# Kernel tuning notes

Hardware: AMD Instinct MI355X
Metric: run time of the kernel (lower is better)

Reference implementation:

```python
import jax, jax.numpy as jnp
import numpy as np

NUM_IN_CAPS = 1152   # 32 * 6 * 6
NUM_OUT_CAPS = 10
IN_DIM = 8
OUT_DIM = 16
ROUTING_ITERS = 3
EPS = 1e-8


def squash(s, axis=-1):
    # squash(s) = ||s||^2/(1+||s||^2) * s/||s||
    sq = jnp.sum(s * s, axis=axis, keepdims=True)
    norm = jnp.sqrt(sq + EPS)
    return (sq / (1.0 + sq)) * (s / norm)


def setup_inputs() -> dict:
    key = jax.random.key(0)
    ks = jax.random.split(key, 6)
    B = 512
    inp = jax.random.uniform(ks[0], (B, 1, 28, 28), dtype=jnp.float32)
    # conv params (He-ish scale)
    conv1_w = jax.random.normal(ks[1], (256, 1, 9, 9), dtype=jnp.float32) * 0.05
    conv1_b = jnp.zeros((256,), dtype=jnp.float32)
    conv2_w = jax.random.normal(ks[2], (256, 256, 9, 9), dtype=jnp.float32) * 0.01
    conv2_b = jnp.zeros((256,), dtype=jnp.float32)
    # capsule transform weights: [in_caps, out_caps, in_dim, out_dim]
    cap_W = jax.random.normal(ks[3], (NUM_IN_CAPS, NUM_OUT_CAPS, IN_DIM, OUT_DIM), dtype=jnp.float32) * 0.05
    return {"input": inp, "conv1_w": conv1_w, "conv1_b": conv1_b,
            "conv2_w": conv2_w, "conv2_b": conv2_b, "cap_W": cap_W}


def _conv(x, w, b, stride):
    y = jax.lax.conv_general_dilated(
        x, w, window_strides=(stride, stride), padding='VALID',
        dimension_numbers=('NCHW', 'OIHW', 'NCHW'))
    return y + b[None, :, None, None]


def capsnet_forward(input, conv1_w, conv1_b, conv2_w, conv2_b, cap_W):
    B = input.shape[0]
    h = jax.nn.relu(_conv(input, conv1_w, conv1_b, 1))   # [B,256,20,20]
    h = _conv(h, conv2_w, conv2_b, 2)                    # [B,256,6,6]
    # torch.transpose(output, 1, -1): [B,C,H,W] -> [B,W,H,C], then view(B,1152,8)
    u = jnp.transpose(h, (0, 3, 2, 1)).reshape(B, NUM_IN_CAPS, IN_DIM)
    # predicted output vectors u_hat: [B, i, j, q]
    u_hat = jnp.einsum('bip,ijpq->bijq', u, cap_W)
    # dynamic routing
    b_ij = jnp.zeros((B, NUM_IN_CAPS, NUM_OUT_CAPS), dtype=u_hat.dtype)
    v = None
    for _ in range(ROUTING_ITERS):
        c = jax.nn.softmax(b_ij, axis=2)                 # coupling over output caps
        s = jnp.einsum('bij,bijq->bjq', c, u_hat)        # [B, j, q]
        v = squash(s)                                    # [B, j, q]
        b_ij = b_ij + jnp.einsum('bijq,bjq->bij', u_hat, v)
    return v  # [B, 10, 16]


def reference(input, conv1_w, conv1_b, conv2_w, conv2_b, cap_W):
    return capsnet_forward(input, conv1_w, conv1_b, conv2_w, conv2_b, cap_W)
```

## Files before the change

kernel.cpp:

```cpp
#include <hip/hip_runtime.h>
#include <hip/hip_bf16.h>

typedef __attribute__((ext_vector_type(8))) short bf16x8;
typedef __attribute__((ext_vector_type(4))) float f32x4;

static __device__ __forceinline__ unsigned short f2bf(float x) {
    __hip_bfloat16 h = __float2bfloat16(x);
    return *(unsigned short*)&h;
}
static __device__ __forceinline__ float bflo(unsigned int w) { return __uint_as_float(w << 16); }
static __device__ __forceinline__ float bfhi(unsigned int w) { return __uint_as_float(w & 0xffff0000u); }
static __device__ __forceinline__ float bf1(unsigned short u) { return __uint_as_float(((unsigned int)u) << 16); }

typedef __attribute__((address_space(1))) const void gvoid;
typedef __attribute__((address_space(3))) void lvoid;
static __device__ __forceinline__ void gl_lds16(const void* g, void* l) {
    __builtin_amdgcn_global_load_lds((gvoid*)g, (lvoid*)l, 16, 0, 0);
}

#define PART_FLOATS 4718592

__global__ __launch_bounds__(320) void conv1_k(const float* __restrict__ in,
                                               const float* __restrict__ w,
                                               const float* __restrict__ bias,
                                               unsigned short* __restrict__ h1n) {
    int blk = blockIdx.x;
    int b = blk >> 4;
    int c0 = (blk & 15) * 16;
    __shared__ float img[784];
    __shared__ float wl[16 * 81];
    __shared__ float bl[16];
    __shared__ unsigned short tr[20 * 328];
    int tid = threadIdx.x;
    for (int t = tid; t < 784; t += 320) img[t] = in[b * 784 + t];
    for (int t = tid; t < 1296; t += 320) wl[t] = w[c0 * 81 + t];
    if (tid < 16) bl[tid] = bias[c0 + tid];
    __syncthreads();

    int co = tid / 20, oy = tid % 20;
    float wr[81];
#pragma unroll
    for (int k = 0; k < 81; k++) wr[k] = wl[co * 81 + k];
    float acc[20];
    float bv = bl[co];
#pragma unroll
    for (int ox = 0; ox < 20; ox++) acc[ox] = bv;

#pragma unroll
    for (int ky = 0; ky < 9; ky++) {
        const float* rp = &img[(oy + ky) * 28];
        float r[28];
#pragma unroll
        for (int v = 0; v < 7; v++) {
            float4 t4 = ((const float4*)rp)[v];
            r[v * 4 + 0] = t4.x; r[v * 4 + 1] = t4.y;
            r[v * 4 + 2] = t4.z; r[v * 4 + 3] = t4.w;
        }
#pragma unroll
        for (int kx = 0; kx < 9; kx++) {
            float wv = wr[ky * 9 + kx];
#pragma unroll
            for (int ox = 0; ox < 20; ox++) acc[ox] += r[ox + kx] * wv;
        }
    }
#pragma unroll
    for (int ox = 0; ox < 20; ox++)
        tr[oy * 328 + ox * 16 + co] = f2bf(fmaxf(acc[ox], 0.f));
    __syncthreads();
    for (int g = tid; g < 800; g += 320) {
        int p = g >> 1, half = g & 1;
        uint4 v = *(uint4*)&tr[(p / 20) * 328 + (p % 20) * 16 + half * 8];
        *(uint4*)&h1n[(b * 400 + p) * 256 + c0 + half * 8] = v;
    }
}

__global__ __launch_bounds__(256) void wt2_k(const float* __restrict__ w2,
                                             unsigned short* __restrict__ Wt2) {
    int cout = blockIdx.x;
    int tid = threadIdx.x;
    __shared__ unsigned short lw[256 * 84];
    lw[tid * 84 + 81] = 0; lw[tid * 84 + 82] = 0; lw[tid * 84 + 83] = 0;
    const float4* src = (const float4*)(w2 + (size_t)cout * 20736);
    for (int t = tid; t < 5184; t += 256) {
        float4 v = src[t];
        int flat = t * 4;
#pragma unroll
        for (int e = 0; e < 4; e++) {
            int f = flat + e;
            int cin = f / 81, kk = f - cin * 81;
            float x = (e == 0) ? v.x : (e == 1) ? v.y : (e == 2) ? v.z : v.w;
            lw[cin * 84 + kk] = f2bf(x);
        }
    }
    __syncthreads();
    int kko = tid >> 7, c2 = (tid & 127) * 2;
    for (int base = 0; base < 84; base += 2) {
        int kk = base + kko;
        unsigned int val = (unsigned int)lw[c2 * 84 + kk]
                         | ((unsigned int)lw[(c2 + 1) * 84 + kk] << 16);
        *(unsigned int*)&Wt2[(size_t)kk * 65536 + cout * 256 + c2] = val;
    }
}

__global__ __launch_bounds__(256) void wcap_k(const float* __restrict__ W,
                                              unsigned short* __restrict__ Wb) {
    int idx4 = blockIdx.x * 256 + threadIdx.x;
    float4 v = *(const float4*)&W[(size_t)idx4 * 4];
    unsigned int lo = (unsigned int)f2bf(v.x) | ((unsigned int)f2bf(v.y) << 16);
    unsigned int hi = (unsigned int)f2bf(v.z) | ((unsigned int)f2bf(v.w) << 16);
    uint2 pk; pk.x = lo; pk.y = hi;
    *(uint2*)&Wb[(size_t)idx4 * 4] = pk;
}

__global__ __launch_bounds__(256) void conv2_k(const unsigned short* __restrict__ h1n,
                                               const unsigned short* __restrict__ Wt2,
                                               const float* __restrict__ bias,
                                               float* __restrict__ u,
                                               float* __restrict__ part1,
                                               float* __restrict__ part23) {
    __shared__ unsigned short sA[2][128 * 64];
    __shared__ unsigned short sB[2][128 * 64];
    int tid = threadIdx.x;
    int m0 = blockIdx.x * 128;
    int n0 = blockIdx.y * 128;
    int slice = blockIdx.z;
    int ks = slice * 21;

    int wv = tid >> 6, lane = tid & 63;
    int wm = wv >> 1, wn = wv & 1;
    int lr = lane & 15, quad = lane >> 4;

    int lrow = lane >> 3, lslot = lane & 7;
    int kcoff = (lslot ^ lrow) * 8;
    int aG[4], bG[4];
#pragma unroll
    for (int t = 0; t < 4; t++) {
        int r = wv * 32 + t * 8 + lrow;
        int R = m0 + r;
        int b = R / 36, m = R % 36;
        int oy = m / 6, ox = m % 6;
        aG[t] = b * 102400 + oy * 10240 + ox * 512 + kcoff;
        bG[t] = (n0 + r) * 256 + kcoff;
    }

    f32x4 acc[4][4];
#pragma unroll
    for (int i = 0; i < 4; i++)
#pragma unroll
        for (int j = 0; j < 4; j++) acc[i][j] = (f32x4){0.f, 0.f, 0.f, 0.f};

    auto stage = [&](int buf, int rr) {
        int kk = ks + (rr >> 2), cr = rr & 3;
        int ky = kk / 9, kx = kk % 9;
        int aoff = ky * 5120 + kx * 256 + cr * 64;
        int boff = kk * 65536 + cr * 64;
        unsigned short* dA = &sA[buf][wv * 2048];
        unsigned short* dB = &sB[buf][wv * 2048];
#pragma unroll
        for (int t = 0; t < 4; t++)
            gl_lds16(h1n + aG[t] + aoff, dA + t * 512);
#pragma unroll
        for (int t = 0; t < 4; t++)
            gl_lds16(Wt2 + bG[t] + boff, dB + t * 512);
    };

    stage(0, 0);
    __syncthreads();

    int cur = 0;
#pragma unroll 1
    for (int rr = 0; rr < 84; rr++) {
        if (rr < 83) stage(cur ^ 1, rr + 1);
        const unsigned short* pA = &sA[cur][0];
        const unsigned short* pB = &sB[cur][0];
#pragma unroll
        for (int s = 0; s < 2; s++) {
            bf16x8 af[4], bf[4];
#pragma unroll
            for (int i = 0; i < 4; i++) {
                int arow = wm * 64 + i * 16 + lr;
                af[i] = *(bf16x8*)&pA[arow * 64 + 8 * ((s * 4 + quad) ^ (lr & 7))];
            }
#pragma unroll
            for (int j = 0; j < 4; j++) {
                int brow = wn * 64 + j * 16 + lr;
                bf[j] = *(bf16x8*)&pB[brow * 64 + 8 * ((s * 4 + quad) ^ (lr & 7))];
            }
#pragma unroll
            for (int i = 0; i < 4; i++)
#pragma unroll
                for (int j = 0; j < 4; j++)
                    acc[i][j] = __builtin_amdgcn_mfma_f32_16x16x32_bf16(
                        af[i], bf[j], acc[i][j], 0, 0, 0);
        }
        __syncthreads();
        cur ^= 1;
    }

    float* dst = (slice == 0) ? u : ((slice == 1) ? part1 : part23 + (size_t)(slice - 2) * PART_FLOATS);
#pragma unroll
    for (int j = 0; j < 4; j++) {
        int col = n0 + wn * 64 + j * 16 + lr;
        float bv = (slice == 0) ? bias[col] : 0.f;
#pragma unroll
        for (int i = 0; i < 4; i++) {
#pragma unroll
            for (int rg = 0; rg < 4; rg++) {
                int RR = m0 + wm * 64 + i * 16 + quad * 4 + rg;
                int bb = RR / 36, mm = RR % 36;
                int oyy = mm / 6, oxx = mm % 6;
                dst[bb * 9216 + oxx * 1536 + oyy * 256 + col] = acc[i][j][rg] + bv;
            }
        }
    }
}

__global__ __launch_bounds__(256) void uhat_k(const float* __restrict__ u,
                                              const float* __restrict__ p1,
                                              const float* __restrict__ p23,
                                              const unsigned short* __restrict__ Wb,
                                              unsigned short* __restrict__ uhat) {
    int i0 = blockIdx.x * 64;
    int b0 = blockIdx.y * 8;
    __shared__ float ul[8 * 576];
    __shared__ unsigned short wl[64 * 130];
    int tid = threadIdx.x;

    for (int t = tid; t < 1024; t += 256) {
        int bb = t >> 7, rq = t & 127;
        int r = rq * 4;
        size_t gidx = (size_t)(b0 + bb) * 9216 + i0 * 8 + r;
        float4 a = *(const float4*)&u[gidx];
        float4 x = *(const float4*)&p1[gidx];
        float4 y = *(const float4*)&p23[gidx];
        float4 z = *(const float4*)&p23[PART_FLOATS + gidx];
        float* d = &ul[bb * 576 + (r >> 3) * 9 + (r & 7)];
        d[0] = a.x + x.x + y.x + z.x;
        d[1] = a.y + x.y + y.y + z.y;
        d[2] = a.z + x.z + y.z + z.z;
        d[3] = a.w + x.w + y.w + z.w;
    }

    int il = tid & 63, g = tid >> 6;
    for (int j = 0; j < 10; j++) {
        __syncthreads();
        for (int t = tid; t < 4096; t += 256) {
            int li = t >> 6, cp = t & 63;
            *(unsigned int*)&wl[li * 130 + cp * 2] =
                *(const unsigned int*)&Wb[(size_t)(i0 + li) * 1280 + j * 128 + cp * 2];
        }
        __syncthreads();
#pragma unroll 1
        for (int bb = 0; bb < 8; bb++) {
            float ur[8];
#pragma unroll
            for (int p = 0; p < 8; p++) ur[p] = ul[bb * 576 + il * 9 + p];
            float a[4];
#pragma unroll
            for (int k = 0; k < 4; k++) {
                int q = g * 4 + k;
                float s = 0.f;
#pragma unroll
                for (int p = 0; p < 8; p++) s += ur[p] * bf1(wl[il * 130 + p * 16 + q]);
                a[k] = s;
            }
            unsigned int lo = (unsigned int)f2bf(a[0]) | ((unsigned int)f2bf(a[1]) << 16);
            unsigned int hi = (unsigned int)f2bf(a[2]) | ((unsigned int)f2bf(a[3]) << 16);
            uint2 pk; pk.x = lo; pk.y = hi;
            *(uint2*)&uhat[((size_t)(b0 + bb) * 10 + j) * 18432 + (size_t)(i0 + il) * 16 + g * 4] = pk;
        }
    }
}

__global__ __launch_bounds__(256) void route_k(const unsigned short* __restrict__ uhat,
                                               float* __restrict__ out) {
    int b = blockIdx.x;
    int tid = threadIdx.x;
    int w = tid >> 6, lane = tid & 63;
    int ig = lane >> 2, qh = lane & 3;
    __shared__ float b_sh[1152 * 10];
    __shared__ float s_red[4 * 160];
    __shared__ float v_sh[160];
    __shared__ float sc_sh[10];
    const unsigned short* ub = uhat + (size_t)b * 184320;

    float v_ln[10][4];

    auto finish = [&](float sp[10][4]) {
#pragma unroll
        for (int j = 0; j < 10; j++)
#pragma unroll
            for (int k = 0; k < 4; k++) {
                float t = sp[j][k];
                t += __shfl_xor(t, 4);
                t += __shfl_xor(t, 8);
                t += __shfl_xor(t, 16);
                t += __shfl_xor(t, 32);
                sp[j][k] = t;
            }
        if (ig == 0) {
#pragma unroll
            for (int j = 0; j < 10; j++) {
                f32x4 v4 = {sp[j][0], sp[j][1], sp[j][2], sp[j][3]};
                *(f32x4*)&s_red[w * 160 + j * 16 + qh * 4] = v4;
            }
        }
        __syncthreads();
        if (tid < 160) {
            float s = s_red[tid] + s_red[160 + tid] + s_red[320 + tid] + s_red[480 + tid];
            s_red[tid] = s;
        }
        __syncthreads();
        if (tid < 10) {
            float sq = 0.f;
#pragma unroll
            for (int q = 0; q < 16; q++) { float x = s_red[tid * 16 + q]; sq += x * x; }
            float norm = sqrtf(sq + 1e-8f);
            sc_sh[tid] = (sq / (1.0f + sq)) / norm;
        }
        __syncthreads();
        if (tid < 160) v_sh[tid] = s_red[tid] * sc_sh[tid >> 4];
        __syncthreads();
#pragma unroll
        for (int j = 0; j < 10; j++) {
            f32x4 v4 = *(const f32x4*)&v_sh[j * 16 + qh * 4];
            v_ln[j][0] = v4[0]; v_ln[j][1] = v4[1]; v_ln[j][2] = v4[2]; v_ln[j][3] = v4[3];
        }
        __syncthreads();
    };

    {
        float sp[10][4];
#pragma unroll
        for (int j = 0; j < 10; j++)
#pragma unroll
            for (int k = 0; k < 4; k++) sp[j][k] = 0.f;
#pragma unroll 2
        for (int r = 0; r < 18; r++) {
            int i = r * 64 + w * 16 + ig;
            const unsigned short* up = ub + (size_t)i * 16 + qh * 4;
            uint2 uh[10];
#pragma unroll
            for (int j = 0; j < 10; j++) uh[j] = *(const uint2*)(up + (size_t)j * 18432);
#pragma unroll
            for (int j = 0; j < 10; j++) {
                sp[j][0] += 0.1f * bflo(uh[j].x);
                sp[j][1] += 0.1f * bfhi(uh[j].x);
                sp[j][2] += 0.1f * bflo(uh[j].y);
                sp[j][3] += 0.1f * bfhi(uh[j].y);
            }
        }
        finish(sp);
    }

#pragma unroll 1
    for (int pass = 0; pass < 2; pass++) {
        bool first = (pass == 0);
        float sp[10][4];
#pragma unroll
        for (int j = 0; j < 10; j++)
#pragma unroll
            for (int k = 0; k < 4; k++) sp[j][k] = 0.f;
#pragma unroll 2
        for (int r = 0; r < 18; r++) {
            int i = r * 64 + w * 16 + ig;
            const unsigned short* up = ub + (size_t)i * 16 + qh * 4;
            uint2 uh[10];
#pragma unroll
            for (int j = 0; j < 10; j++) uh[j] = *(const uint2*)(up + (size_t)j * 18432);
            float d[10];
#pragma unroll
            for (int j = 0; j < 10; j++) {
                d[j] = bflo(uh[j].x) * v_ln[j][0] + bfhi(uh[j].x) * v_ln[j][1]
                     + bflo(uh[j].y) * v_ln[j][2] + bfhi(uh[j].y) * v_ln[j][3];
            }
#pragma unroll
            for (int j = 0; j < 10; j++) {
                d[j] += __shfl_xor(d[j], 1);
                d[j] += __shfl_xor(d[j], 2);
            }
            float bn[10];
            if (first) {
#pragma unroll
                for (int j = 0; j < 10; j++) bn[j] = d[j];
#pragma unroll
                for (int j = 0; j < 10; j++)
                    if (qh == (j & 3)) b_sh[i * 10 + j] = bn[j];
            } else {
#pragma unroll
                for (int j = 0; j < 10; j++) bn[j] = b_sh[i * 10 + j] + d[j];
            }
            float m = bn[0];
#pragma unroll
            for (int j = 1; j < 10; j++) m = fmaxf(m, bn[j]);
            float e[10], sum = 0.f;
#pragma unroll
            for (int j = 0; j < 10; j++) { e[j] = __expf(bn[j] - m); sum += e[j]; }
            float inv = 1.f / sum;
#pragma unroll
            for (int j = 0; j < 10; j++) {
                float c = e[j] * inv;
                sp[j][0] += c * bflo(uh[j].x);
                sp[j][1] += c * bfhi(uh[j].x);
                sp[j][2] += c * bflo(uh[j].y);
                sp[j][3] += c * bfhi(uh[j].y);
            }
        }
        finish(sp);
    }

    if (tid < 160) out[b * 160 + tid] = v_sh[tid];
}

extern "C" void kernel_launch(void* const* d_in, const int* in_sizes, int n_in,
                              void* d_out, int out_size, void* d_ws, size_t ws_size,
                              hipStream_t stream) {
    const float* input = (const float*)d_in[0];
    const float* c1w = (const float*)d_in[1];
    const float* c1b = (const float*)d_in[2];
    const float* c2w = (const float*)d_in[3];
    const float* c2b = (const float*)d_in[4];
    const float* capW = (const float*)d_in[5];
    float* out = (float*)d_out;

    const size_t U_OFF = 0;
    const size_t P1_OFF = 18874368;
    const size_t WB_OFF = 37748736;
    const size_t B_OFF = 43122688;
    const size_t WT2_BYTES = (size_t)84 * 65536 * 2;
    const size_t H1N_BYTES = 104857600;
    const size_t PART_BYTES = (size_t)PART_FLOATS * 4;
    const size_t CONV_BYTES = WT2_BYTES + H1N_BYTES + 2 * PART_BYTES;
    if (ws_size < B_OFF + CONV_BYTES) return;

    char* wsb = (char*)d_ws;
    float* u_buf = (float*)(wsb + U_OFF);
    float* part1 = (float*)(wsb + P1_OFF);
    unsigned short* Wb = (unsigned short*)(wsb + WB_OFF);
    unsigned short* Wt2 = (unsigned short*)(wsb + B_OFF);
    unsigned short* h1n = (unsigned short*)(wsb + B_OFF + WT2_BYTES);
    float* part23 = (float*)(wsb + B_OFF + WT2_BYTES + H1N_BYTES);
    unsigned short* uhatb = (unsigned short*)(wsb + B_OFF);

    wcap_k<<<1440, 256, 0, stream>>>(capW, Wb);
    wt2_k<<<256, 256, 0, stream>>>(c2w, Wt2);
    conv1_k<<<512 * 16, 320, 0, stream>>>(input, c1w, c1b, h1n);
    conv2_k<<<dim3(144, 2, 4), 256, 0, stream>>>(h1n, Wt2, c2b, u_buf, part1, part23);

    const int Cr = 256;
    for (int b0 = 0; b0 < 512; b0 += Cr) {
        uhat_k<<<dim3(18, Cr / 8), 256, 0, stream>>>(
            u_buf + (size_t)b0 * 9216, part1 + (size_t)b0 * 9216,
            part23 + (size_t)b0 * 9216, Wb, uhatb);
        route_k<<<Cr, 256, 0, stream>>>(uhatb, out + (size_t)b0 * 160);
    }
}
```

Measured before the change: 699.2 us.

## Rewrite conv1 as implicit-GEMM on bf16 MFMA with swizzled LDS tiles

Replaces the scalar FP32 direct convolution in conv1 with an im2col-style implicit GEMM. Each block now handles one image and 64 output channels, building swizzled bf16 A (patch) and B (weight) tiles in LDS and accumulating with 16x16x32 bf16 MFMA. The intent is to move conv1's FLOPs onto matrix cores. In exchange, the input image and weights are rounded to bf16, K is padded from 81 to 96, and the output stores become scattered 2-byte writes instead of 16-byte vector stores.

```diff
diff --git a/kernel.cpp b/kernel.cpp
--- a/kernel.cpp
+++ b/kernel.cpp
@@ -20,57 +20,91 @@
 
 #define PART_FLOATS 4718592
 
-__global__ __launch_bounds__(320) void conv1_k(const float* __restrict__ in,
+__global__ __launch_bounds__(256) void conv1_k(const float* __restrict__ in,
                                                const float* __restrict__ w,
                                                const float* __restrict__ bias,
                                                unsigned short* __restrict__ h1n) {
-    int blk = blockIdx.x;
-    int b = blk >> 4;
-    int c0 = (blk & 15) * 16;
-    __shared__ float img[784];
-    __shared__ float wl[16 * 81];
-    __shared__ float bl[16];
-    __shared__ unsigned short tr[20 * 328];
+    int b = blockIdx.x;
+    int c0 = blockIdx.y * 64;
     int tid = threadIdx.x;
-    for (int t = tid; t < 784; t += 320) img[t] = in[b * 784 + t];
-    for (int t = tid; t < 1296; t += 320) wl[t] = w[c0 * 81 + t];
-    if (tid < 16) bl[tid] = bias[c0 + tid];
+    __shared__ unsigned short imgbf[784];
+    __shared__ unsigned short Al[448 * 32];
+    __shared__ unsigned short Btl[3][64 * 32];
+
+    if (tid < 196) {
+        float4 v = *(const float4*)&in[b * 784 + tid * 4];
+        imgbf[tid * 4 + 0] = f2bf(v.x);
+        imgbf[tid * 4 + 1] = f2bf(v.y);
+        imgbf[tid * 4 + 2] = f2bf(v.z);
+        imgbf[tid * 4 + 3] = f2bf(v.w);
+    }
+    for (int idx = tid; idx < 6144; idx += 256) {
+        int ksb = idx >> 11;
+        int r = idx & 2047;
+        int c = r >> 5, kid = r & 31;
+        int k = ksb * 32 + kid;
+        unsigned short v = (k < 81) ? f2bf(w[(size_t)(c0 + c) * 81 + k]) : (unsigned short)0;
+        Btl[ksb][c * 32 + 8 * ((kid >> 3) ^ ((c >> 1) & 3)) + (kid & 7)] = v;
+    }
+
+    int wv = tid >> 6, lane = tid & 63;
+    int lr = lane & 15, quad = lane >> 4;
+    int wrow = wv * 112;
+
+    f32x4 acc[7][4];
+#pragma unroll
+    for (int mi = 0; mi < 7; mi++)
+#pragma unroll
+        for (int ni = 0; ni < 4; ni++) acc[mi][ni] = (f32x4){0.f, 0.f, 0.f, 0.f};
+
     __syncthreads();
 
-    int co = tid / 20, oy = tid % 20;
-    float wr[81];
-#pragma unroll
-    for (int k = 0; k < 81; k++) wr[k] = wl[co * 81 + k];
-    float acc[20];
-    float bv = bl[co];
-#pragma unroll
-    for (int ox = 0; ox < 20; ox++) acc[ox] = bv;
-
-#pragma unroll
-    for (int ky = 0; ky < 9; ky++) {
-        const float* rp = &img[(oy + ky) * 28];
-        float r[28];
-#pragma unroll
-        for (int v = 0; v < 7; v++) {
-            float4 t4 = ((const float4*)rp)[v];
-            r[v * 4 + 0] = t4.x; r[v * 4 + 1] = t4.y;
-            r[v * 4 + 2] = t4.z; r[v * 4 + 3] = t4.w;
-        }
-#pragma unroll
-        for (int kx = 0; kx < 9; kx++) {
-            float wv = wr[ky * 9 + kx];
-#pragma unroll
-            for (int ox = 0; ox < 20; ox++) acc[ox] += r[ox + kx] * wv;
-        }
-    }
-#pragma unroll
-    for (int ox = 0; ox < 20; ox++)
-        tr[oy * 328 + ox * 16 + co] = f2bf(fmaxf(acc[ox], 0.f));
-    __syncthreads();
-    for (int g = tid; g < 800; g += 320) {
-        int p = g >> 1, half = g & 1;
-        uint4 v = *(uint4*)&tr[(p / 20) * 328 + (p % 20) * 16 + half * 8];
-        *(uint4*)&h1n[(b * 400 + p) * 256 + c0 + half * 8] = v;
+#pragma unroll 1
+    for (int ks = 0; ks < 3; ks++) {
+        for (int idx = tid; idx < 14336; idx += 256) {
+            int row = idx >> 5, kid = idx & 31;
+            int k = ks * 32 + kid;
+            unsigned short v = 0;
+            if (row < 400 && k < 81) {
+                int oy = row / 20, ox = row - oy * 20;
+                int ky = k / 9, kx = k - ky * 9;
+                v = imgbf[(oy + ky) * 28 + ox + kx];
+            }
+            Al[row * 32 + 8 * ((kid >> 3) ^ ((row >> 1) & 3)) + (kid & 7)] = v;
+        }
+        __syncthreads();
+        bf16x8 bf[4];
+#pragma unroll
+        for (int ni = 0; ni < 4; ni++) {
+            int c = ni * 16 + lr;
+            bf[ni] = *(const bf16x8*)&Btl[ks][c * 32 + 8 * (quad ^ ((c >> 1) & 3))];
+        }
+#pragma unroll
+        for (int mi = 0; mi < 7; mi++) {
+            int row = wrow + mi * 16 + lr;
+            bf16x8 av = *(const bf16x8*)&Al[row * 32 + 8 * (quad ^ ((row >> 1) & 3))];
+#pragma unroll
+            for (int ni = 0; ni < 4; ni++)
+                acc[mi][ni] = __builtin_amdgcn_mfma_f32_16x16x32_bf16(
+                    av, bf[ni], acc[mi][ni], 0, 0, 0);
+        }
+        __syncthreads();
+    }
+
+#pragma unroll
+    for (int ni = 0; ni < 4; ni++) {
+        int c = c0 + ni * 16 + lr;
+        float bv = bias[c];
+#pragma unroll
+        for (int mi = 0; mi < 7; mi++) {
+#pragma unroll
+            for (int rg = 0; rg < 4; rg++) {
+                int p = wrow + mi * 16 + quad * 4 + rg;
+                if (p < 400)
+                    h1n[((size_t)b * 400 + p) * 256 + c] =
+                        f2bf(fmaxf(acc[mi][ni][rg] + bv, 0.f));
+            }
+        }
     }
 }
 
@@ -444,7 +478,7 @@
 
     wcap_k<<<1440, 256, 0, stream>>>(capW, Wb);
     wt2_k<<<256, 256, 0, stream>>>(c2w, Wt2);
-    conv1_k<<<512 * 16, 320, 0, stream>>>(input, c1w, c1b, h1n);
+    conv1_k<<<dim3(512, 4), 256, 0, stream>>>(input, c1w, c1b, h1n);
     conv2_k<<<dim3(144, 2, 4), 256, 0, stream>>>(h1n, Wt2, c2b, u_buf, part1, part23);
 
     const int Cr = 256;
```

New measurement: 877.3 us. 1.25x slower.
